# Kernel optimization log

Hardware: AMD Instinct MI355X
Metric: run time of the kernel (lower is better)

## Reference

```python
import jax, jax.numpy as jnp
import numpy as np

N_NODES = 200_000
N_EDGES = 6_400_000
N_GRAPHS = 512


def _graph_conv(x, src, dst, W_rel, b_rel, W_root, n_nodes):
    # PyG GraphConv (aggr='add'): lin_rel(sum_{j->i} x_j) + lin_root(x_i)
    agg = jax.ops.segment_sum(x[src], dst, num_segments=n_nodes)  # [N, in]
    return agg @ W_rel.T + b_rel + x @ W_root.T


def setup_inputs() -> dict:
    key = jax.random.key(0)
    ks = jax.random.split(key, 12)
    x = jax.random.normal(ks[0], (N_NODES, 3), dtype=jnp.float32)
    edge_index = jax.random.randint(ks[1], (2, N_EDGES), 0, N_NODES, dtype=jnp.int64)
    batch = jnp.sort(jax.random.randint(ks[2], (N_NODES,), 0, N_GRAPHS, dtype=jnp.int64))

    def xavier(k, shape):
        fan_out, fan_in = shape
        lim = np.sqrt(6.0 / (fan_in + fan_out)).astype(np.float32)
        return jax.random.uniform(k, shape, jnp.float32, -lim, lim)

    return {
        "x": x, "edge_index": edge_index, "batch": batch,
        "W1_rel": xavier(ks[3], (32, 3)),  "b1": jnp.zeros((32,), jnp.float32), "W1_root": xavier(ks[4], (32, 3)),
        "W2_rel": xavier(ks[5], (16, 32)), "b2": jnp.zeros((16,), jnp.float32), "W2_root": xavier(ks[6], (16, 32)),
        "W3_rel": xavier(ks[7], (8, 16)),  "b3": jnp.zeros((8,), jnp.float32),  "W3_root": xavier(ks[8], (8, 16)),
        "W_lin": xavier(ks[9], (1, 8)),    "b_lin": jnp.zeros((1,), jnp.float32),
    }


def reference(x, edge_index, batch,
              W1_rel, b1, W1_root,
              W2_rel, b2, W2_root,
              W3_rel, b3, W3_root,
              W_lin, b_lin):
    src, dst = edge_index[0], edge_index[1]
    h = jax.nn.relu(_graph_conv(x, src, dst, W1_rel, b1, W1_root, N_NODES))
    h = jax.nn.relu(_graph_conv(h, src, dst, W2_rel, b2, W2_root, N_NODES))
    h = jax.nn.relu(_graph_conv(h, src, dst, W3_rel, b3, W3_root, N_NODES))
    pooled = jax.ops.segment_max(h, batch, num_segments=N_GRAPHS)  # [G, 8]
    out = pooled @ W_lin.T + b_lin  # [G, 1]
    return out[:, 0]
```

## Files before the change

### kernel.cpp

```cpp
#include <hip/hip_runtime.h>
#include <hip/hip_fp16.h>

#define N_NODES 200000
#define N_EDGES 6400000
#define N_GRAPHS 512

#define NB1 196
#define CB 1024
#define NSB 16
#define NFB (NB1 * NSB)
#define CHUNK 8192
#define NCH 782
#define NGRP 25
#define CPG 32
#define SCAP 3072
#define NBLK32 (N_NODES / 32)

typedef float vf4 __attribute__((ext_vector_type(4)));
typedef float vf2 __attribute__((ext_vector_type(2)));
typedef unsigned vu2 __attribute__((ext_vector_type(2)));

__device__ __forceinline__ unsigned ntload_u(const unsigned* p) {
  return __builtin_nontemporal_load(p);
}
__device__ __forceinline__ int ntload_i(const int* p) { return __builtin_nontemporal_load(p); }
__device__ __forceinline__ float ntload_f(const float* p) {
  return __builtin_nontemporal_load(p);
}
__device__ __forceinline__ float2 ntload_f2(const float* p) {
  vf2 v = __builtin_nontemporal_load((const vf2*)p);
  return make_float2(v.x, v.y);
}
__device__ __forceinline__ void ntstore_f2(float* p, float2 v) {
  vf2 t = {v.x, v.y};
  __builtin_nontemporal_store(t, (vf2*)p);
}
__device__ __forceinline__ void ntstore_u(unsigned* p, unsigned v) {
  __builtin_nontemporal_store(v, p);
}


__global__ __launch_bounds__(256) void count_kernel(const int* __restrict__ dst,
                                                    unsigned short* __restrict__ H) {
  __shared__ unsigned hist[4][NB1];
  int t = threadIdx.x, w = t >> 6;
  for (int i = t; i < 4 * NB1; i += 256) ((unsigned*)hist)[i] = 0;
  __syncthreads();
  int c = blockIdx.x;
  long e0 = (long)c * CHUNK;
  long rem = (long)N_EDGES - e0;
  int n = rem > CHUNK ? CHUNK : (int)rem;
  for (int i = t; i < n; i += 256) atomicAdd(&hist[w][dst[e0 + i] >> 10], 1u);
  __syncthreads();
  for (int b = t; b < NB1; b += 256)
    H[(size_t)c * NB1 + b] =
        (unsigned short)(hist[0][b] + hist[1][b] + hist[2][b] + hist[3][b]);
}

__global__ __launch_bounds__(256) void scan_bins1_kernel(unsigned short* __restrict__ H,
                                                         unsigned* __restrict__ P) {
  int b = blockIdx.x * 256 + threadIdx.x;
  int g = blockIdx.y;
  if (b >= NB1) return;
  int c0 = g * CPG, c1 = min(NCH, (g + 1) * CPG);
  unsigned run = 0;
  for (int c = c0; c < c1; c++) {
    unsigned t = H[(size_t)c * NB1 + b];
    H[(size_t)c * NB1 + b] = (unsigned short)run;
    run += t;
  }
  P[(size_t)g * NB1 + b] = run;
}

__global__ __launch_bounds__(256) void scan_bins2_kernel(unsigned* __restrict__ P,
                                                         unsigned* __restrict__ bucketTotal) {
  int b = blockIdx.x * 256 + threadIdx.x;
  if (b >= NB1) return;
  unsigned run = 0;
  for (int g = 0; g < NGRP; g++) {
    unsigned t = P[(size_t)g * NB1 + b];
    P[(size_t)g * NB1 + b] = run;
    run += t;
  }
  bucketTotal[b] = run;
}

__global__ __launch_bounds__(256) void scan_total_kernel(const unsigned* __restrict__ bucketTotal,
                                                         unsigned* __restrict__ bucketStart) {
  __shared__ unsigned partial[256];
  int t = threadIdx.x;
  unsigned v = (t < NB1) ? bucketTotal[t] : 0u;
  partial[t] = v;
  __syncthreads();
  for (int off = 1; off < 256; off <<= 1) {
    unsigned add = (t >= off) ? partial[t - off] : 0u;
    __syncthreads();
    partial[t] += add;
    __syncthreads();
  }
  if (t < NB1) bucketStart[t] = partial[t] - v;
  if (t == 0) bucketStart[NB1] = N_EDGES;
}

__global__ __launch_bounds__(256) void scatterA_kernel(
    const int* __restrict__ src, const int* __restrict__ dst,
    const unsigned short* __restrict__ H, const unsigned* __restrict__ P,
    const unsigned* __restrict__ bucketStart, unsigned* __restrict__ X1) {
  __shared__ unsigned ssort[CHUNK];
  __shared__ unsigned char sbort[CHUNK];
  __shared__ unsigned histw[4][NB1];
  __shared__ unsigned curw[4][NB1];
  __shared__ unsigned gbase[NB1];
  __shared__ unsigned partial[256];
  int t = threadIdx.x, w = t >> 6;
  int c = blockIdx.x;
  int g = c / CPG;
  long e0 = (long)c * CHUNK;
  long rem = (long)N_EDGES - e0;
  int n = rem > CHUNK ? CHUNK : (int)rem;
  for (int i = t; i < 4 * NB1; i += 256) ((unsigned*)histw)[i] = 0;
  __syncthreads();
  for (int i = t; i < n; i += 256) atomicAdd(&histw[w][dst[e0 + i] >> 10], 1u);
  __syncthreads();
  unsigned tot = 0, h0 = 0, h1 = 0, h2 = 0, h3 = 0;
  if (t < NB1) {
    h0 = histw[0][t]; h1 = histw[1][t]; h2 = histw[2][t]; h3 = histw[3][t];
    tot = h0 + h1 + h2 + h3;
  }
  partial[t] = tot;
  __syncthreads();
  for (int off = 1; off < 256; off <<= 1) {
    unsigned add = (t >= off) ? partial[t - off] : 0u;
    __syncthreads();
    partial[t] += add;
    __syncthreads();
  }
  if (t < NB1) {
    unsigned ex = partial[t] - tot;
    unsigned r = ex;
    curw[0][t] = r; r += h0;
    curw[1][t] = r; r += h1;
    curw[2][t] = r; r += h2;
    curw[3][t] = r;
    gbase[t] = bucketStart[t] + P[(size_t)g * NB1 + t] + (unsigned)H[(size_t)c * NB1 + t] - ex;
  }
  __syncthreads();
  for (int i = t; i < n; i += 256) {
    int d = dst[e0 + i], s = src[e0 + i];
    int b = d >> 10;
    unsigned r = atomicAdd(&curw[w][b], 1u);
    ssort[r] = ((unsigned)s << 10) | (unsigned)(d & 1023);
    sbort[r] = (unsigned char)b;
  }
  __syncthreads();
  for (int j = t; j < n; j += 256) X1[gbase[sbort[j]] + j] = ssort[j];
}

__global__ __launch_bounds__(1024) void scatterB_kernel(
    const unsigned* __restrict__ X1, const unsigned* __restrict__ bucketStart,
    unsigned* __restrict__ X2, unsigned* __restrict__ fineStart) {
  __shared__ unsigned histw[16][NSB];
  __shared__ unsigned binstart[NSB + 1];
  __shared__ unsigned cur[NSB];
  int t = threadIdx.x, w = t >> 6, b = blockIdx.x;
  unsigned cs0 = bucketStart[b], cs1 = bucketStart[b + 1];
  int n = (int)(cs1 - cs0);
  if (t < 16 * NSB) ((unsigned*)histw)[t] = 0;
  __syncthreads();
  for (int i = t; i < n; i += 1024)
    atomicAdd(&histw[w][(X1[cs0 + i] >> 6) & 15u], 1u);
  __syncthreads();
  if (t == 0) {
    unsigned run = 0;
    for (int k = 0; k < NSB; k++) {
      binstart[k] = run;
      unsigned tot = 0;
      for (int ww = 0; ww < 16; ww++) tot += histw[ww][k];
      run += tot;
    }
    binstart[NSB] = run;
  }
  __syncthreads();
  if (t < NSB) {
    fineStart[b * NSB + t] = cs0 + binstart[t];
    cur[t] = binstart[t];
  }
  if (b == NB1 - 1 && t == 0) fineStart[NFB] = cs1;
  __syncthreads();
  for (int i = t; i < n; i += 1024) {
    unsigned v = X1[cs0 + i];
    unsigned pos = atomicAdd(&cur[(v >> 6) & 15u], 1u);
    X2[cs0 + pos] = v;
  }
}

__global__ __launch_bounds__(256) void sort2_kernel(const unsigned* __restrict__ X2,
                                                    const unsigned* __restrict__ fineStart,
                                                    unsigned* __restrict__ packedB,
                                                    unsigned* __restrict__ nodeStart) {
  __shared__ unsigned buf[SCAP];
  __shared__ unsigned buf2[SCAP];
  __shared__ unsigned hist[64], base[64], cur[64];
  int t = threadIdx.x, b = blockIdx.x;
  unsigned s0 = fineStart[b], s1 = fineStart[b + 1];
  int n = (int)(s1 - s0);
  if (t < 64) hist[t] = 0;
  for (int i = t; i < n; i += 256) buf[i] = ntload_u(&X2[s0 + i]);
  __syncthreads();
  for (int i = t; i < n; i += 256) atomicAdd(&hist[buf[i] & 63u], 1u);
  __syncthreads();
  if (t == 0) {
    unsigned run = 0;
    for (int k = 0; k < 64; k++) {
      unsigned v = hist[k];
      base[k] = run;
      cur[k] = run;
      run += v;
    }
  }
  __syncthreads();
  if (t < 64) {
    int gn = b * 64 + t;
    if (gn <= N_NODES) nodeStart[gn] = s0 + base[t];
  }
  for (int i = t; i < n; i += 256) {
    unsigned p = buf[i];
    unsigned pos = atomicAdd(&cur[p & 63u], 1u);
    buf2[pos] = p >> 10;
  }
  __syncthreads();
  for (int i = t; i < n; i += 256) ntstore_u(&packedB[s0 + i], buf2[i]);
}

__global__ __launch_bounds__(256) void xpad_kernel(const float* __restrict__ x,
                                                   float4* __restrict__ xp) {
  int n = blockIdx.x * 256 + threadIdx.x;
  if (n >= N_NODES) return;
  xp[n] = make_float4(x[3 * n], x[3 * n + 1], x[3 * n + 2], 0.f);
}

__device__ __forceinline__ void half8_unpack(uint4 g, float* f) {
  const __half2* h2 = reinterpret_cast<const __half2*>(&g);
#pragma unroll
  for (int j = 0; j < 4; j++) {
    float2 fj = __half22float2(h2[j]);
    f[2 * j] = fj.x;
    f[2 * j + 1] = fj.y;
  }
}

__global__ __launch_bounds__(256) void layer1a_kernel(
    const unsigned* __restrict__ packed, const unsigned* __restrict__ nodeStart,
    const float4* __restrict__ xp, float* __restrict__ agg) {
  __shared__ float plds[256 * 9];
  int t = threadIdx.x, ln = t >> 3, p = t & 7;
  int node = blockIdx.x * 32 + ln;
  unsigned s1v = ntload_u(&nodeStart[node + 1]);
  float a0 = 0.f, a1 = 0.f, a2 = 0.f;
  for (unsigned base = ntload_u(&nodeStart[node]) + p; base < s1v; base += 32) {
    unsigned i1 = base + 8, i2 = base + 16, i3 = base + 24;
    unsigned e0 = ntload_u(&packed[base]);
    unsigned e1 = ntload_u(&packed[i1]);
    unsigned e2 = ntload_u(&packed[i2]);
    unsigned e3 = ntload_u(&packed[i3]);
    float4 g0 = xp[e0], g1 = xp[e1], g2 = xp[e2], g3 = xp[e3];
    float m1 = (i1 < s1v) ? 1.f : 0.f;
    float m2 = (i2 < s1v) ? 1.f : 0.f;
    float m3 = (i3 < s1v) ? 1.f : 0.f;
    a0 += g0.x + m1 * g1.x + m2 * g2.x + m3 * g3.x;
    a1 += g0.y + m1 * g1.y + m2 * g2.y + m3 * g3.y;
    a2 += g0.z + m1 * g1.z + m2 * g2.z + m3 * g3.z;
  }
  plds[t * 9] = a0; plds[t * 9 + 1] = a1; plds[t * 9 + 2] = a2;
  __syncthreads();
  if (p < 4) {
    int q0 = ln * 72 + p;
    float v = 0.f;
    if (p < 3)
      v = plds[q0] + plds[q0 + 9] + plds[q0 + 18] + plds[q0 + 27] +
          plds[q0 + 36] + plds[q0 + 45] + plds[q0 + 54] + plds[q0 + 63];
    agg[(size_t)node * 4 + p] = v;
  }
}

__global__ __launch_bounds__(256) void layer1b_kernel(
    const float4* __restrict__ xp, const float4* __restrict__ agg,
    const float* __restrict__ W1_rel, const float* __restrict__ b1,
    const float* __restrict__ W1_root,
    const float* __restrict__ W2_rel, const float* __restrict__ W2_root,
    uint4* __restrict__ t2h4, float4* __restrict__ r24) {
  __shared__ float sW1rel[96], sW1root[96], sb1[32], sW2rel[512], sW2root[512];
  for (int i = threadIdx.x; i < 96; i += 256) { sW1rel[i] = W1_rel[i]; sW1root[i] = W1_root[i]; }
  for (int i = threadIdx.x; i < 32; i += 256) sb1[i] = b1[i];
  for (int i = threadIdx.x; i < 512; i += 256) { sW2rel[i] = W2_rel[i]; sW2root[i] = W2_root[i]; }
  __syncthreads();
  int node = blockIdx.x * 256 + threadIdx.x;
  if (node >= N_NODES) return;
  float4 A = agg[node];
  float4 xv = xp[node];
  float h[32];
#pragma unroll
  for (int k = 0; k < 32; k++) {
    float v = sW1rel[3 * k] * A.x + sW1rel[3 * k + 1] * A.y + sW1rel[3 * k + 2] * A.z +
              sW1root[3 * k] * xv.x + sW1root[3 * k + 1] * xv.y + sW1root[3 * k + 2] * xv.z +
              sb1[k];
    h[k] = fmaxf(v, 0.f);
  }
  unsigned tp[8];
#pragma unroll
  for (int j = 0; j < 16; j += 2) {
    float t0 = 0.f, t1 = 0.f;
#pragma unroll
    for (int k = 0; k < 32; k++) {
      t0 += sW2rel[32 * j + k] * h[k];
      t1 += sW2rel[32 * (j + 1) + k] * h[k];
    }
    __half2 pk = __halves2half2(__float2half_rn(t0), __float2half_rn(t1));
    tp[j >> 1] = *(unsigned*)&pk;
  }
  t2h4[(size_t)node * 2] = make_uint4(tp[0], tp[1], tp[2], tp[3]);
  t2h4[(size_t)node * 2 + 1] = make_uint4(tp[4], tp[5], tp[6], tp[7]);
#pragma unroll
  for (int q = 0; q < 4; q++) {
    float rv[4];
#pragma unroll
    for (int jj = 0; jj < 4; jj++) {
      int j = 4 * q + jj;
      float a = 0.f;
#pragma unroll
      for (int k = 0; k < 32; k++) a += sW2root[32 * j + k] * h[k];
      rv[jj] = a;
    }
    r24[(size_t)node * 4 + q] = make_float4(rv[0], rv[1], rv[2], rv[3]);
  }
}

__global__ __launch_bounds__(256) void layer2g_kernel(
    const unsigned* __restrict__ packed, const unsigned* __restrict__ nodeStart,
    const uint4* __restrict__ t2h4, __half* __restrict__ agg2, int half) {
  __shared__ float plds[256 * 9];
  int t = threadIdx.x, ln = t >> 3, p = t & 7;
  int node = blockIdx.x * 32 + ln;
  unsigned s1v = ntload_u(&nodeStart[node + 1]);
  float acc[8];
#pragma unroll
  for (int j = 0; j < 8; j++) acc[j] = 0.f;
  for (unsigned base = ntload_u(&nodeStart[node]) + p; base < s1v; base += 32) {
    unsigned i1 = base + 8, i2 = base + 16, i3 = base + 24;
    unsigned e0 = ntload_u(&packed[base]);
    unsigned e1 = ntload_u(&packed[i1]);
    unsigned e2 = ntload_u(&packed[i2]);
    unsigned e3 = ntload_u(&packed[i3]);
    uint4 g0 = t2h4[(size_t)e0 * 2 + half];
    uint4 g1 = t2h4[(size_t)e1 * 2 + half];
    uint4 g2 = t2h4[(size_t)e2 * 2 + half];
    uint4 g3 = t2h4[(size_t)e3 * 2 + half];
    float m1 = (i1 < s1v) ? 1.f : 0.f;
    float m2 = (i2 < s1v) ? 1.f : 0.f;
    float m3 = (i3 < s1v) ? 1.f : 0.f;
    float f0[8], f1[8], f2[8], f3[8];
    half8_unpack(g0, f0);
    half8_unpack(g1, f1);
    half8_unpack(g2, f2);
    half8_unpack(g3, f3);
#pragma unroll
    for (int j = 0; j < 8; j++)
      acc[j] += f0[j] + m1 * f1[j] + m2 * f2[j] + m3 * f3[j];
  }
#pragma unroll
  for (int j = 0; j < 8; j++) plds[t * 9 + j] = acc[j];
  __syncthreads();
  int q0 = ln * 72 + p;
  float s = plds[q0] + plds[q0 + 9] + plds[q0 + 18] + plds[q0 + 27] +
            plds[q0 + 36] + plds[q0 + 45] + plds[q0 + 54] + plds[q0 + 63];
  agg2[(size_t)node * 16 + half * 8 + p] = __float2half_rn(s);
}

__global__ __launch_bounds__(256) void layer2e_kernel(
    const uint4* agg2q, const float4* __restrict__ r24,
    const float* __restrict__ b2, const float* __restrict__ W3_rel,
    const float* __restrict__ W3_root, uint4* __restrict__ t3h4, float4* r34) {
  __shared__ float sW3rel[128], sW3root[128], sb2[16];
  for (int i = threadIdx.x; i < 128; i += 256) { sW3rel[i] = W3_rel[i]; sW3root[i] = W3_root[i]; }
  if (threadIdx.x < 16) sb2[threadIdx.x] = b2[threadIdx.x];
  __syncthreads();
  int node = blockIdx.x * 256 + threadIdx.x;
  if (node >= N_NODES) return;
  uint4 ga = agg2q[(size_t)node * 2];
  uint4 gb = agg2q[(size_t)node * 2 + 1];
  float ag[16];
  half8_unpack(ga, ag);
  half8_unpack(gb, ag + 8);
  float h[16];
#pragma unroll
  for (int q = 0; q < 4; q++) {
    float4 rv = r24[(size_t)node * 4 + q];
    h[4 * q] = fmaxf(ag[4 * q] + rv.x + sb2[4 * q], 0.f);
    h[4 * q + 1] = fmaxf(ag[4 * q + 1] + rv.y + sb2[4 * q + 1], 0.f);
    h[4 * q + 2] = fmaxf(ag[4 * q + 2] + rv.z + sb2[4 * q + 2], 0.f);
    h[4 * q + 3] = fmaxf(ag[4 * q + 3] + rv.w + sb2[4 * q + 3], 0.f);
  }
  unsigned tp[4];
#pragma unroll
  for (int j = 0; j < 8; j += 2) {
    float t0 = 0.f, t1 = 0.f;
#pragma unroll
    for (int k = 0; k < 16; k++) {
      t0 += sW3rel[16 * j + k] * h[k];
      t1 += sW3rel[16 * (j + 1) + k] * h[k];
    }
    __half2 pk = __halves2half2(__float2half_rn(t0), __float2half_rn(t1));
    tp[j >> 1] = *(unsigned*)&pk;
  }
  t3h4[node] = make_uint4(tp[0], tp[1], tp[2], tp[3]);
  float rv[8];
#pragma unroll
  for (int j = 0; j < 8; j++) {
    float a = 0.f;
#pragma unroll
    for (int k = 0; k < 16; k++) a += sW3root[16 * j + k] * h[k];
    rv[j] = a;
  }
  r34[(size_t)node * 2] = make_float4(rv[0], rv[1], rv[2], rv[3]);
  r34[(size_t)node * 2 + 1] = make_float4(rv[4], rv[5], rv[6], rv[7]);
}

__global__ __launch_bounds__(256) void layer3_kernel(
    const unsigned* __restrict__ packed, const unsigned* __restrict__ nodeStart,
    const uint4* __restrict__ t3h4, const float* __restrict__ r3,
    const float* __restrict__ b3,
    const int* __restrict__ batch, unsigned* __restrict__ pooled) {
  __shared__ float plds[256 * 9];
  __shared__ float sb3[8];
  __shared__ int sgid[32];
  if (threadIdx.x < 8) sb3[threadIdx.x] = b3[threadIdx.x];
  __syncthreads();
  int t = threadIdx.x, ln = t >> 3, p = t & 7;
  int node = blockIdx.x * 32 + ln;
  unsigned s1v = ntload_u(&nodeStart[node + 1]);
  float acc[8];
#pragma unroll
  for (int j = 0; j < 8; j++) acc[j] = 0.f;
  for (unsigned base = ntload_u(&nodeStart[node]) + p; base < s1v; base += 32) {
    unsigned i1 = base + 8, i2 = base + 16, i3 = base + 24;
    unsigned e0 = ntload_u(&packed[base]);
    unsigned e1 = ntload_u(&packed[i1]);
    unsigned e2 = ntload_u(&packed[i2]);
    unsigned e3 = ntload_u(&packed[i3]);
    uint4 g0 = t3h4[e0];
    uint4 g1 = t3h4[e1];
    uint4 g2 = t3h4[e2];
    uint4 g3 = t3h4[e3];
    float m1 = (i1 < s1v) ? 1.f : 0.f;
    float m2 = (i2 < s1v) ? 1.f : 0.f;
    float m3 = (i3 < s1v) ? 1.f : 0.f;
    float f0[8], f1[8], f2[8], f3[8];
    half8_unpack(g0, f0);
    half8_unpack(g1, f1);
    half8_unpack(g2, f2);
    half8_unpack(g3, f3);
#pragma unroll
    for (int j = 0; j < 8; j++)
      acc[j] += f0[j] + m1 * f1[j] + m2 * f2[j] + m3 * f3[j];
  }
#pragma unroll
  for (int j = 0; j < 8; j++) plds[t * 9 + j] = acc[j];
  __syncthreads();
  int gg = ntload_i(&batch[node]);
  int q0 = ln * 72 + p;
  float v = plds[q0] + plds[q0 + 9] + plds[q0 + 18] + plds[q0 + 27] +
            plds[q0 + 36] + plds[q0 + 45] + plds[q0 + 54] + plds[q0 + 63];
  float h = fmaxf(v + sb3[p] + ntload_f(&r3[(size_t)node * 8 + p]), 0.f);
  __syncthreads();
  plds[ln * 9 + p] = h;
  if (p == 0) sgid[ln] = gg;
  __syncthreads();
  if (t < 8) {
    int gcur = sgid[0];
    float m = plds[t];
    for (int l = 1; l < 32; l++) {
      int g2 = sgid[l];
      float hv = plds[l * 9 + t];
      if (g2 != gcur) {
        atomicMax(&pooled[8 * gcur + t], __float_as_uint(m));
        gcur = g2;
        m = hv;
      } else {
        m = fmaxf(m, hv);
      }
    }
    atomicMax(&pooled[8 * gcur + t], __float_as_uint(m));
  }
}

__global__ __launch_bounds__(256) void final_kernel(
    const unsigned* __restrict__ pooled, const float* __restrict__ W_lin,
    const float* __restrict__ b_lin, float* __restrict__ out) {
  int g = blockIdx.x * blockDim.x + threadIdx.x;
  if (g >= N_GRAPHS) return;
  float acc = b_lin[0];
#pragma unroll
  for (int f = 0; f < 8; f++) acc += __uint_as_float(pooled[8 * g + f]) * W_lin[f];
  out[g] = acc;
}

extern "C" void kernel_launch(void* const* d_in, const int* in_sizes, int n_in,
                              void* d_out, int out_size, void* d_ws, size_t ws_size,
                              hipStream_t stream) {
  const float* x = (const float*)d_in[0];
  const int* ei = (const int*)d_in[1];
  const int* src = ei;
  const int* dst = ei + N_EDGES;
  const int* batch = (const int*)d_in[2];
  const float* W1_rel = (const float*)d_in[3];
  const float* b1 = (const float*)d_in[4];
  const float* W1_root = (const float*)d_in[5];
  const float* W2_rel = (const float*)d_in[6];
  const float* b2 = (const float*)d_in[7];
  const float* W2_root = (const float*)d_in[8];
  const float* W3_rel = (const float*)d_in[9];
  const float* b3 = (const float*)d_in[10];
  const float* W3_root = (const float*)d_in[11];
  const float* W_lin = (const float*)d_in[12];
  const float* b_lin = (const float*)d_in[13];
  float* out = (float*)d_out;

  char* ws = (char*)d_ws;
  unsigned* X2 = (unsigned*)(ws + 0);
  float* r2 = (float*)(ws + 0);
  float* agg = (float*)(ws + 12800000);
  __half* agg2 = (__half*)(ws + 12800000);
  float* r3 = (float*)(ws + 12800000);
  unsigned* t3h = (unsigned*)(ws + 19200000);
  float4* xpad = (float4*)(ws + 22400000);
  unsigned* X1 = (unsigned*)(ws + 25600000);
  unsigned* packedB = (unsigned*)(ws + 25600000);
  unsigned* t2h = (unsigned*)(ws + 51200128);
  unsigned short* H = (unsigned short*)(ws + 51200128);
  unsigned* P = (unsigned*)(ws + 51506672);
  unsigned* bucketTotal = (unsigned*)(ws + 51526272);
  unsigned* bucketStart = (unsigned*)(ws + 51527056);
  unsigned* fineStart = (unsigned*)(ws + 51527844);
  unsigned* pooled = (unsigned*)(ws + 57600128);
  unsigned* nodeStart = (unsigned*)(ws + 57954016);

  hipMemsetAsync(pooled, 0, N_GRAPHS * 8 * sizeof(unsigned), stream);
  hipMemsetAsync(packedB + N_EDGES, 0, 128, stream);

  count_kernel<<<NCH, 256, 0, stream>>>(dst, H);
  scan_bins1_kernel<<<dim3((NB1 + 255) / 256, NGRP), 256, 0, stream>>>(H, P);
  scan_bins2_kernel<<<(NB1 + 255) / 256, 256, 0, stream>>>(P, bucketTotal);
  scan_total_kernel<<<1, 256, 0, stream>>>(bucketTotal, bucketStart);
  scatterA_kernel<<<NCH, 256, 0, stream>>>(src, dst, H, P, bucketStart, X1);
  scatterB_kernel<<<NB1, 1024, 0, stream>>>(X1, bucketStart, X2, fineStart);
  sort2_kernel<<<NFB, 256, 0, stream>>>(X2, fineStart, packedB, nodeStart);
  xpad_kernel<<<(N_NODES + 255) / 256, 256, 0, stream>>>(x, xpad);

  layer1a_kernel<<<NBLK32, 256, 0, stream>>>(packedB, nodeStart, xpad, agg);
  layer1b_kernel<<<(N_NODES + 255) / 256, 256, 0, stream>>>(
      xpad, (const float4*)agg, W1_rel, b1, W1_root, W2_rel, W2_root,
      (uint4*)t2h, (float4*)r2);

  layer2g_kernel<<<NBLK32, 256, 0, stream>>>(packedB, nodeStart, (const uint4*)t2h, agg2, 0);
  layer2g_kernel<<<NBLK32, 256, 0, stream>>>(packedB, nodeStart, (const uint4*)t2h, agg2, 1);
  layer2e_kernel<<<(N_NODES + 255) / 256, 256, 0, stream>>>(
      (const uint4*)agg2, (const float4*)r2, b2, W3_rel, W3_root,
      (uint4*)t3h, (float4*)r3);

  layer3_kernel<<<N_NODES / 32, 256, 0, stream>>>(packedB, nodeStart, (const uint4*)t3h, r3, b3,
                                                  batch, pooled);
  final_kernel<<<(N_GRAPHS + 255) / 256, 256, 0, stream>>>(pooled, W_lin, b_lin, out);
}
```

Baseline: 488.5 us.

## Split layer-2 gather by source-node half instead of feature half

```diff
diff --git a/kernel.cpp b/kernel.cpp
--- a/kernel.cpp
+++ b/kernel.cpp
@@ -4,15 +4,16 @@
 #define N_NODES 200000
 #define N_EDGES 6400000
 #define N_GRAPHS 512
+#define HALFN 100000
 
 #define NB1 196
 #define CB 1024
 #define NSB 16
 #define NFB (NB1 * NSB)
-#define CHUNK 8192
-#define NCH 782
+#define CHUNK 4096
+#define NCH 1563
 #define NGRP 25
-#define CPG 32
+#define CPG 63
 #define SCAP 3072
 #define NBLK32 (N_NODES / 32)
 
@@ -27,18 +28,9 @@
 __device__ __forceinline__ float ntload_f(const float* p) {
   return __builtin_nontemporal_load(p);
 }
-__device__ __forceinline__ float2 ntload_f2(const float* p) {
-  vf2 v = __builtin_nontemporal_load((const vf2*)p);
-  return make_float2(v.x, v.y);
-}
-__device__ __forceinline__ void ntstore_f2(float* p, float2 v) {
-  vf2 t = {v.x, v.y};
-  __builtin_nontemporal_store(t, (vf2*)p);
-}
 __device__ __forceinline__ void ntstore_u(unsigned* p, unsigned v) {
   __builtin_nontemporal_store(v, p);
 }
-
 
 __global__ __launch_bounds__(256) void count_kernel(const int* __restrict__ dst,
                                                     unsigned short* __restrict__ H) {
@@ -197,21 +189,26 @@
 __global__ __launch_bounds__(256) void sort2_kernel(const unsigned* __restrict__ X2,
                                                     const unsigned* __restrict__ fineStart,
                                                     unsigned* __restrict__ packedB,
-                                                    unsigned* __restrict__ nodeStart) {
+                                                    unsigned* __restrict__ nodeStart,
+                                                    unsigned char* __restrict__ deltaSplit) {
   __shared__ unsigned buf[SCAP];
   __shared__ unsigned buf2[SCAP];
-  __shared__ unsigned hist[64], base[64], cur[64];
+  __shared__ unsigned hist[128], base[128], cur[128];
   int t = threadIdx.x, b = blockIdx.x;
   unsigned s0 = fineStart[b], s1 = fineStart[b + 1];
   int n = (int)(s1 - s0);
-  if (t < 64) hist[t] = 0;
+  if (t < 128) hist[t] = 0;
   for (int i = t; i < n; i += 256) buf[i] = ntload_u(&X2[s0 + i]);
   __syncthreads();
-  for (int i = t; i < n; i += 256) atomicAdd(&hist[buf[i] & 63u], 1u);
+  for (int i = t; i < n; i += 256) {
+    unsigned v = buf[i];
+    unsigned bin = ((v & 63u) << 1) | ((v >> 10) >= HALFN ? 1u : 0u);
+    atomicAdd(&hist[bin], 1u);
+  }
   __syncthreads();
   if (t == 0) {
     unsigned run = 0;
-    for (int k = 0; k < 64; k++) {
+    for (int k = 0; k < 128; k++) {
       unsigned v = hist[k];
       base[k] = run;
       cur[k] = run;
@@ -221,12 +218,14 @@
   __syncthreads();
   if (t < 64) {
     int gn = b * 64 + t;
-    if (gn <= N_NODES) nodeStart[gn] = s0 + base[t];
+    if (gn <= N_NODES) nodeStart[gn] = s0 + base[2 * t];
+    if (gn < N_NODES) deltaSplit[gn] = (unsigned char)(base[2 * t + 1] - base[2 * t]);
   }
   for (int i = t; i < n; i += 256) {
-    unsigned p = buf[i];
-    unsigned pos = atomicAdd(&cur[p & 63u], 1u);
-    buf2[pos] = p >> 10;
+    unsigned v = buf[i];
+    unsigned bin = ((v & 63u) << 1) | ((v >> 10) >= HALFN ? 1u : 0u);
+    unsigned pos = atomicAdd(&cur[bin], 1u);
+    buf2[pos] = v >> 10;
   }
   __syncthreads();
   for (int i = t; i < n; i += 256) ntstore_u(&packedB[s0 + i], buf2[i]);
@@ -337,43 +336,54 @@
 
 __global__ __launch_bounds__(256) void layer2g_kernel(
     const unsigned* __restrict__ packed, const unsigned* __restrict__ nodeStart,
-    const uint4* __restrict__ t2h4, __half* __restrict__ agg2, int half) {
-  __shared__ float plds[256 * 9];
+    const unsigned char* __restrict__ deltaSplit,
+    const uint4* __restrict__ t2h4, __half* __restrict__ agg2, int pass) {
+  __shared__ float plds[256 * 17];
   int t = threadIdx.x, ln = t >> 3, p = t & 7;
   int node = blockIdx.x * 32 + ln;
-  unsigned s1v = ntload_u(&nodeStart[node + 1]);
-  float acc[8];
-#pragma unroll
-  for (int j = 0; j < 8; j++) acc[j] = 0.f;
-  for (unsigned base = ntload_u(&nodeStart[node]) + p; base < s1v; base += 32) {
-    unsigned i1 = base + 8, i2 = base + 16, i3 = base + 24;
+  unsigned s0n = ntload_u(&nodeStart[node]);
+  unsigned s1n = ntload_u(&nodeStart[node + 1]);
+  unsigned split = s0n + (unsigned)deltaSplit[node];
+  unsigned lo = pass ? split : s0n;
+  unsigned hi = pass ? s1n : split;
+  float acc[16];
+#pragma unroll
+  for (int j = 0; j < 16; j++) acc[j] = 0.f;
+  for (unsigned base = lo + p; base < hi; base += 16) {
+    unsigned i1 = base + 8;
     unsigned e0 = ntload_u(&packed[base]);
-    unsigned e1 = ntload_u(&packed[i1]);
-    unsigned e2 = ntload_u(&packed[i2]);
-    unsigned e3 = ntload_u(&packed[i3]);
-    uint4 g0 = t2h4[(size_t)e0 * 2 + half];
-    uint4 g1 = t2h4[(size_t)e1 * 2 + half];
-    uint4 g2 = t2h4[(size_t)e2 * 2 + half];
-    uint4 g3 = t2h4[(size_t)e3 * 2 + half];
-    float m1 = (i1 < s1v) ? 1.f : 0.f;
-    float m2 = (i2 < s1v) ? 1.f : 0.f;
-    float m3 = (i3 < s1v) ? 1.f : 0.f;
-    float f0[8], f1[8], f2[8], f3[8];
-    half8_unpack(g0, f0);
-    half8_unpack(g1, f1);
-    half8_unpack(g2, f2);
-    half8_unpack(g3, f3);
-#pragma unroll
-    for (int j = 0; j < 8; j++)
-      acc[j] += f0[j] + m1 * f1[j] + m2 * f2[j] + m3 * f3[j];
-  }
-#pragma unroll
-  for (int j = 0; j < 8; j++) plds[t * 9 + j] = acc[j];
-  __syncthreads();
-  int q0 = ln * 72 + p;
-  float s = plds[q0] + plds[q0 + 9] + plds[q0 + 18] + plds[q0 + 27] +
-            plds[q0 + 36] + plds[q0 + 45] + plds[q0 + 54] + plds[q0 + 63];
-  agg2[(size_t)node * 16 + half * 8 + p] = __float2half_rn(s);
+    unsigned e1r = ntload_u(&packed[i1]);
+    bool in1 = i1 < hi;
+    unsigned e1 = in1 ? e1r : e0;
+    uint4 g0a = t2h4[(size_t)e0 * 2], g0b = t2h4[(size_t)e0 * 2 + 1];
+    uint4 g1a = t2h4[(size_t)e1 * 2], g1b = t2h4[(size_t)e1 * 2 + 1];
+    float f0[16], f1[16];
+    half8_unpack(g0a, f0);
+    half8_unpack(g0b, f0 + 8);
+    half8_unpack(g1a, f1);
+    half8_unpack(g1b, f1 + 8);
+    float m1 = in1 ? 1.f : 0.f;
+#pragma unroll
+    for (int j = 0; j < 16; j++) acc[j] += f0[j] + m1 * f1[j];
+  }
+#pragma unroll
+  for (int j = 0; j < 16; j++) plds[t * 17 + j] = acc[j];
+  __syncthreads();
+  int qb = ln * 8 * 17;
+  float s0 = 0.f, s1 = 0.f;
+#pragma unroll
+  for (int k = 0; k < 8; k++) {
+    s0 += plds[qb + k * 17 + 2 * p];
+    s1 += plds[qb + k * 17 + 2 * p + 1];
+  }
+  __half* dst = &agg2[(size_t)node * 16 + 2 * p];
+  if (pass) {
+    __half2 old = *(const __half2*)dst;
+    float2 of = __half22float2(old);
+    s0 += of.x;
+    s1 += of.y;
+  }
+  *(__half2*)dst = __halves2half2(__float2half_rn(s0), __float2half_rn(s1));
 }
 
 __global__ __launch_bounds__(256) void layer2e_kernel(
@@ -537,11 +547,12 @@
   unsigned* packedB = (unsigned*)(ws + 25600000);
   unsigned* t2h = (unsigned*)(ws + 51200128);
   unsigned short* H = (unsigned short*)(ws + 51200128);
-  unsigned* P = (unsigned*)(ws + 51506672);
-  unsigned* bucketTotal = (unsigned*)(ws + 51526272);
-  unsigned* bucketStart = (unsigned*)(ws + 51527056);
-  unsigned* fineStart = (unsigned*)(ws + 51527844);
+  unsigned* P = (unsigned*)(ws + 51812824);
+  unsigned* bucketTotal = (unsigned*)(ws + 51832424);
+  unsigned* bucketStart = (unsigned*)(ws + 51833208);
+  unsigned* fineStart = (unsigned*)(ws + 51833996);
   unsigned* pooled = (unsigned*)(ws + 57600128);
+  unsigned char* deltaSplit = (unsigned char*)(ws + 57616512);
   unsigned* nodeStart = (unsigned*)(ws + 57954016);
 
   hipMemsetAsync(pooled, 0, N_GRAPHS * 8 * sizeof(unsigned), stream);
@@ -553,7 +564,7 @@
   scan_total_kernel<<<1, 256, 0, stream>>>(bucketTotal, bucketStart);
   scatterA_kernel<<<NCH, 256, 0, stream>>>(src, dst, H, P, bucketStart, X1);
   scatterB_kernel<<<NB1, 1024, 0, stream>>>(X1, bucketStart, X2, fineStart);
-  sort2_kernel<<<NFB, 256, 0, stream>>>(X2, fineStart, packedB, nodeStart);
+  sort2_kernel<<<NFB, 256, 0, stream>>>(X2, fineStart, packedB, nodeStart, deltaSplit);
   xpad_kernel<<<(N_NODES + 255) / 256, 256, 0, stream>>>(x, xpad);
 
   layer1a_kernel<<<NBLK32, 256, 0, stream>>>(packedB, nodeStart, xpad, agg);
@@ -561,13 +572,15 @@
       xpad, (const float4*)agg, W1_rel, b1, W1_root, W2_rel, W2_root,
       (uint4*)t2h, (float4*)r2);
 
-  layer2g_kernel<<<NBLK32, 256, 0, stream>>>(packedB, nodeStart, (const uint4*)t2h, agg2, 0);
-  layer2g_kernel<<<NBLK32, 256, 0, stream>>>(packedB, nodeStart, (const uint4*)t2h, agg2, 1);
+  layer2g_kernel<<<NBLK32, 256, 0, stream>>>(packedB, nodeStart, deltaSplit,
+                                             (const uint4*)t2h, agg2, 0);
+  layer2g_kernel<<<NBLK32, 256, 0, stream>>>(packedB, nodeStart, deltaSplit,
+                                             (const uint4*)t2h, agg2, 1);
   layer2e_kernel<<<(N_NODES + 255) / 256, 256, 0, stream>>>(
       (const uint4*)agg2, (const float4*)r2, b2, W3_rel, W3_root,
       (uint4*)t3h, (float4*)r3);
 
-  layer3_kernel<<<N_NODES / 32, 256, 0, stream>>>(packedB, nodeStart, (const uint4*)t3h, r3, b3,
-                                                  batch, pooled);
+  layer3_kernel<<<NBLK32, 256, 0, stream>>>(packedB, nodeStart, (const uint4*)t3h, r3, b3,
+                                            batch, pooled);
   final_kernel<<<(N_GRAPHS + 255) / 256, 256, 0, stream>>>(pooled, W_lin, b_lin, out);
 }
```

Result: faster. 425.0 us (-13.0%).
